# Kernel optimization log

Measured on AMD Instinct MI355X. Metric: run time of the kernel, lower is better.

## Reference

```python
import jax, jax.numpy as jnp
import numpy as np

B, S, D = 2, 2048, 2048
H, KVH, HD = 16, 4, 128
E, TOPK, FF = 8, 2, 4096
EPS = 1e-6
THETA = 1000000.0


def setup_inputs() -> dict:
    key = jax.random.key(0)
    ks = jax.random.split(key, 12)
    s = 0.02
    return {
        'hidden_states': jax.random.normal(ks[0], (B, S, D), jnp.float32),
        'attention_mask': jnp.ones((B, S), dtype=bool),
        'wq': jax.random.normal(ks[1], (D, H * HD), jnp.float32) * s,
        'wk': jax.random.normal(ks[2], (D, KVH * HD), jnp.float32) * s,
        'wv': jax.random.normal(ks[3], (D, KVH * HD), jnp.float32) * s,
        'wo': jax.random.normal(ks[4], (H * HD, D), jnp.float32) * s,
        'ln1_w': jnp.ones((D,), jnp.float32),
        'ln2_w': jnp.ones((D,), jnp.float32),
        'gate_w': jax.random.normal(ks[5], (D, E), jnp.float32) * s,
        'w_gate': jax.random.normal(ks[6], (E, D, FF), jnp.float32) * s,
        'w_up': jax.random.normal(ks[7], (E, D, FF), jnp.float32) * s,
        'w_down': jax.random.normal(ks[8], (E, FF, D), jnp.float32) * s,
    }


def rms_norm(x, w):
    xf = x.astype(jnp.float32)
    var = jnp.mean(jnp.square(xf), axis=-1, keepdims=True)
    return w * (xf * jax.lax.rsqrt(var + EPS)).astype(x.dtype)


def rotate_half(x):
    x1, x2 = x[..., : x.shape[-1] // 2], x[..., x.shape[-1] // 2 :]
    return jnp.concatenate((-x2, x1), axis=-1)


def attention(x, mask, wq, wk, wv, wo):
    q = (x @ wq).reshape(B, S, H, HD)
    k = (x @ wk).reshape(B, S, KVH, HD)
    v = (x @ wv).reshape(B, S, KVH, HD)
    # RoPE (fp32 freqs, as in MixtralRotaryEmbedding)
    inv_freq = 1.0 / (THETA ** (jnp.arange(0, HD, 2, dtype=jnp.float32) / HD))
    freqs = jnp.arange(S, dtype=jnp.float32)[:, None] * inv_freq[None, :]  # [S, HD/2]
    emb = jnp.concatenate([freqs, freqs], axis=-1)  # [S, HD]
    cos = jnp.cos(emb)[None, :, None, :]  # [1,S,1,HD]
    sin = jnp.sin(emb)[None, :, None, :]
    q = q * cos + rotate_half(q) * sin
    k = k * cos + rotate_half(k) * sin
    # GQA: repeat kv heads
    k = jnp.repeat(k, H // KVH, axis=2)
    v = jnp.repeat(v, H // KVH, axis=2)
    # faithful to source: keep-mask is triu(ones, k=1) (strictly-above-diagonal)
    causal = jnp.triu(jnp.ones((S, S), dtype=bool), k=1)
    combined = mask[:, None, None, :] & causal[None, None, :, :]  # [B,1,S,S]
    neg = jnp.finfo(jnp.float32).min
    bias = jnp.where(combined, 0.0, neg).astype(jnp.float32)
    scores = jnp.einsum('bqhd,bkhd->bhqk', q, k) * (HD ** -0.5) + bias
    attn = jax.nn.softmax(scores, axis=-1)
    out = jnp.einsum('bhqk,bkhd->bqhd', attn, v).reshape(B, S, H * HD)
    return out @ wo


def moe(x, gate_w, w_gate, w_up, w_down):
    # x: [T, D]
    T = x.shape[0]
    logits = x.astype(jnp.float32) @ gate_w  # fp32 router, [T, E]
    rw = jax.nn.softmax(logits, axis=-1)
    top_w, top_i = jax.lax.top_k(rw, TOPK)
    top_w = top_w / jnp.sum(top_w, axis=-1, keepdims=True)
    w_full = jnp.zeros((T, E), jnp.float32).at[jnp.arange(T)[:, None], top_i].set(top_w)
    out = jnp.zeros_like(x)
    for e in range(E):  # small fixed expert loop
        h = jax.nn.silu(x @ w_gate[e]) * (x @ w_up[e])
        out = out + w_full[:, e, None] * (h @ w_down[e])
    return out


def reference(hidden_states, attention_mask, wq, wk, wv, wo, ln1_w, ln2_w, gate_w, w_gate, w_up, w_down):
    residual = hidden_states
    h = rms_norm(hidden_states, ln1_w)
    h = residual + attention(h, attention_mask, wq, wk, wv, wo)
    residual = h
    h = rms_norm(h, ln2_w)
    m = moe(h.reshape(-1, D), gate_w, w_gate, w_up, w_down).reshape(B, S, D)
    return residual + m
```

## Files before the change

### kernel.cpp

```cpp
#include <hip/hip_runtime.h>
#include <cstdint>
#include <cstddef>


typedef unsigned short u16;
typedef __attribute__((ext_vector_type(8))) short short8;
typedef __attribute__((ext_vector_type(8))) _Float16 half8;
typedef __attribute__((ext_vector_type(8))) __bf16 bf16x8;
typedef __attribute__((ext_vector_type(4))) float f32x4;
typedef __attribute__((ext_vector_type(4))) u16 us4;
typedef __attribute__((ext_vector_type(4))) unsigned int u32x4;

__device__ __forceinline__ u16 f2bf(float f) {
  unsigned u = __builtin_bit_cast(unsigned, f);
  u += 0x7fffu + ((u >> 16) & 1u);
  return (u16)(u >> 16);
}
__device__ __forceinline__ void splitf16(float x, float scale, u16 &hi, u16 &lo) {
  float xs = x * scale;
  _Float16 h = (_Float16)xs;
  hi = __builtin_bit_cast(u16, h);
  _Float16 l = (_Float16)(xs - (float)h);
  lo = __builtin_bit_cast(u16, l);
}
__device__ __forceinline__ f32x4 mma_bf(short8 a, short8 b, f32x4 c) {
  return __builtin_amdgcn_mfma_f32_16x16x32_bf16(
      __builtin_bit_cast(bf16x8, a), __builtin_bit_cast(bf16x8, b), c, 0, 0, 0);
}
__device__ __forceinline__ f32x4 mma_h(short8 a, short8 b, f32x4 c) {
  return __builtin_amdgcn_mfma_f32_16x16x32_f16(
      __builtin_bit_cast(half8, a), __builtin_bit_cast(half8, b), c, 0, 0, 0);
}
__device__ __forceinline__ void gl16(const u16 *g, u16 *l) {
  __builtin_amdgcn_global_load_lds(
      (const __attribute__((address_space(1))) unsigned *)g,
      (__attribute__((address_space(3))) unsigned *)l, 16, 0, 0);
}

template <int OM>
__global__ __launch_bounds__(256) void k_trans(
    const float *__restrict__ src, u16 *__restrict__ d0, u16 *__restrict__ d1,
    int ld_src, int ld_dst, long long zhi, long long zlo, int zmod,
    long long dstz, int inter, float scale) {
  int z = blockIdx.z;
  src += (long long)(z / zmod) * zhi + (long long)(z % zmod) * zlo;
  d0 += (long long)z * dstz;
  if constexpr (OM == 1) d1 += (long long)z * dstz;
  int r0 = blockIdx.y * 64, c0 = blockIdx.x * 64;
  __shared__ float t[64][65];
  int tx = threadIdx.x;
  int rr = tx >> 4, cc = (tx & 15) * 4;
#pragma unroll
  for (int i = 0; i < 4; i++) {
    float4 v = *(const float4 *)(src + (size_t)(r0 + rr + i * 16) * ld_src + c0 + cc);
    t[rr + i * 16][cc] = v.x; t[rr + i * 16][cc + 1] = v.y;
    t[rr + i * 16][cc + 2] = v.z; t[rr + i * 16][cc + 3] = v.w;
  }
  __syncthreads();
#pragma unroll
  for (int i = 0; i < 4; i++) {
    int c = rr + i * 16;
    int f = c0 + c;
    int drow = (inter < 0) ? f : (((f >> 5) << 6) + (f & 31) + (inter << 5));
    size_t bo = (size_t)drow * ld_dst + r0 + cc;
    if constexpr (OM == 0) {
      us4 o;
#pragma unroll
      for (int j = 0; j < 4; j++) o[j] = f2bf(t[cc + j][c]);
      *(us4 *)(d0 + bo) = o;
    } else {
      us4 oh, ol;
#pragma unroll
      for (int j = 0; j < 4; j++) {
        u16 a, b; splitf16(t[cc + j][c], scale, a, b);
        oh[j] = a; ol[j] = b;
      }
      *(us4 *)(d0 + bo) = oh;
      *(us4 *)(d1 + bo) = ol;
    }
  }
}

__global__ __launch_bounds__(256) void k_rms(
    const float *__restrict__ x, const float *__restrict__ w,
    u16 *__restrict__ oh, u16 *__restrict__ ol, float scale16) {
  int row = blockIdx.x, tid = threadIdx.x;
  const float *xr = x + (size_t)row * 2048;
  float4 v0 = *(const float4 *)(xr + tid * 8);
  float4 v1 = *(const float4 *)(xr + tid * 8 + 4);
  float ss = v0.x * v0.x + v0.y * v0.y + v0.z * v0.z + v0.w * v0.w +
             v1.x * v1.x + v1.y * v1.y + v1.z * v1.z + v1.w * v1.w;
  __shared__ float red[256];
  red[tid] = ss;
  __syncthreads();
  for (int s = 128; s > 0; s >>= 1) {
    if (tid < s) red[tid] += red[tid + s];
    __syncthreads();
  }
  float sc = rsqrtf(red[0] * (1.0f / 2048.0f) + 1e-6f);
  float4 w0 = *(const float4 *)(w + tid * 8);
  float4 w1 = *(const float4 *)(w + tid * 8 + 4);
  float o[8] = {v0.x * sc * w0.x, v0.y * sc * w0.y, v0.z * sc * w0.z, v0.w * sc * w0.w,
                v1.x * sc * w1.x, v1.y * sc * w1.y, v1.z * sc * w1.z, v1.w * sc * w1.w};
  size_t bo = (size_t)row * 2048 + tid * 8;
  if (ol) {
    us4 h0, h1, l0, l1;
#pragma unroll
    for (int j = 0; j < 4; j++) {
      u16 a, b;
      splitf16(o[j], scale16, a, b); h0[j] = a; l0[j] = b;
      splitf16(o[j + 4], scale16, a, b); h1[j] = a; l1[j] = b;
    }
    *(us4 *)(oh + bo) = h0; *(us4 *)(oh + bo + 4) = h1;
    *(us4 *)(ol + bo) = l0; *(us4 *)(ol + bo + 4) = l1;
  } else {
    us4 a, b;
#pragma unroll
    for (int j = 0; j < 4; j++) { a[j] = f2bf(o[j]); b[j] = f2bf(o[j + 4]); }
    *(us4 *)(oh + bo) = a; *(us4 *)(oh + bo + 4) = b;
  }
}

__global__ void k_cs(float2 *__restrict__ cs) {
  int idx = blockIdx.x * 256 + threadIdx.x;
  int s = idx >> 6, i = idx & 63;
  double inv = exp2(-(double)i * (19.931568569324174 / 64.0));
  double ang = (double)s * inv;
  cs[idx] = make_float2((float)cos(ang), (float)sin(ang));
}

__global__ __launch_bounds__(256) void k_rope(
    const float *__restrict__ qkv, const float2 *__restrict__ cs,
    u16 *__restrict__ qh, u16 *__restrict__ ql,
    u16 *__restrict__ kh, u16 *__restrict__ kl) {
  int t = blockIdx.x, tid = threadIdx.x;
  int s = t & 2047;
  const float *bp = qkv + (size_t)t * 3072;
  for (int p = tid; p < 1024; p += 256) {
    int hh = p >> 6, i = p & 63;
    float2 c = cs[s * 64 + i];
    float x1 = bp[hh * 128 + i], x2 = bp[hh * 128 + 64 + i];
    float o1 = x1 * c.x - x2 * c.y, o2 = x2 * c.x + x1 * c.y;
    size_t b1 = (size_t)t * 2048 + hh * 128 + i;
    u16 a, b;
    splitf16(o1, 16.f, a, b); qh[b1] = a; ql[b1] = b;
    splitf16(o2, 16.f, a, b); qh[b1 + 64] = a; ql[b1 + 64] = b;
  }
  {
    int hh = tid >> 6, i = tid & 63;
    float2 c = cs[s * 64 + i];
    float x1 = bp[2048 + hh * 128 + i], x2 = bp[2048 + hh * 128 + 64 + i];
    float o1 = x1 * c.x - x2 * c.y, o2 = x2 * c.x + x1 * c.y;
    size_t b1 = (size_t)t * 512 + hh * 128 + i;
    u16 a, b;
    splitf16(o1, 16.f, a, b); kh[b1] = a; kl[b1] = b;
    splitf16(o2, 16.f, a, b); kh[b1 + 64] = a; kl[b1 + 64] = b;
  }
}

__global__ __launch_bounds__(512, 4) void k_attn(
    const u16 *__restrict__ qh, const u16 *__restrict__ ql,
    const u16 *__restrict__ kh, const u16 *__restrict__ kl,
    const u16 *__restrict__ vh, const u16 *__restrict__ vl,
    u16 *__restrict__ oh, u16 *__restrict__ ol) {
  const int qx = blockIdx.x, kvh = blockIdx.y, b = blockIdx.z;
  const int qt = (b == 0) ? qx : 63 - qx;
  const int q0 = qt * 32;
  const int tid = threadIdx.x, wid = tid >> 6, lane = tid & 63;
  const int hq = wid & 3, rh = wid >> 2;
  const int h = kvh * 4 + hq;
  const int lr = lane & 15, g = lane >> 4, lk = g * 8;
  const float SC = 0.08838834764831845f * 1.44269504088896341f / 256.0f;

  __shared__ alignas(16) u16 KT[2][2][4096];
  __shared__ alignas(16) u16 VT[2][2][4096];
  __shared__ alignas(16) u16 Pb[8][2][512];

  short8 qfh[4], qfl[4];
  {
    size_t qo = (size_t)(b * 2048 + q0 + rh * 16 + lr) * 2048 + h * 128 + lk;
#pragma unroll
    for (int c = 0; c < 4; c++) {
      qfh[c] = *(const short8 *)(qh + qo + c * 32);
      qfl[c] = *(const short8 *)(ql + qo + c * 32);
    }
  }
  f32x4 accO[8] = {};
  float m_r[4], l_r[4];
#pragma unroll
  for (int r = 0; r < 4; r++) { m_r[r] = -3.0e38f; l_r[r] = 0.f; }

  const int kv_start = q0;
  const int nIter = (2048 - kv_start) >> 5;

  const u16 *khp = kh + (size_t)(b * 2048) * 512 + kvh * 128;
  const u16 *klp = kl + (size_t)(b * 2048) * 512 + kvh * 128;
  const u16 *vhp = vh + ((size_t)(b * 4 + kvh) * 128) * 2048;
  const u16 *vlp = vl + ((size_t)(b * 4 + kvh) * 128) * 2048;

  auto stage = [&](int bf, int kv0) {
    const int c0 = wid * 64;
    const int cc = tid;
    const int krow = cc >> 4, kcol = (cc & 15) ^ (krow & 7);
    const size_t kg = (size_t)(kv0 + krow) * 512 + kcol * 8;
    gl16(khp + kg, &KT[bf][0][c0 * 8]);
    gl16(klp + kg, &KT[bf][1][c0 * 8]);
    const int vd = cc >> 2, vi = (cc & 3) ^ (vd & 3);
    const size_t vg = (size_t)vd * 2048 + kv0 + vi * 8;
    gl16(vhp + vg, &VT[bf][0][c0 * 8]);
    gl16(vlp + vg, &VT[bf][1][c0 * 8]);
  };

  stage(0, kv_start);
  __syncthreads();
  int buf = 0;
  for (int it = 0; it < nIter; it++) {
    const int kv0 = kv_start + (it << 5);
    if (it + 1 < nIter) stage(buf ^ 1, kv0 + 32);
    f32x4 s0 = {}, s1 = {};
    {
      const u16 *KhL = KT[buf][0], *KlL = KT[buf][1];
#pragma unroll
      for (int c = 0; c < 4; c++) {
        const int idx0 = lr * 128 + (((c * 4 + g) ^ (lr & 7)) << 3);
        const int idx1 = idx0 + 2048;
        short8 k0h = *(const short8 *)(KhL + idx0);
        short8 k0l = *(const short8 *)(KlL + idx0);
        short8 k1h = *(const short8 *)(KhL + idx1);
        short8 k1l = *(const short8 *)(KlL + idx1);
        s0 = mma_h(qfh[c], k0h, s0); s0 = mma_h(qfh[c], k0l, s0); s0 = mma_h(qfl[c], k0h, s0);
        s1 = mma_h(qfh[c], k1h, s1); s1 = mma_h(qfh[c], k1l, s1); s1 = mma_h(qfl[c], k1h, s1);
      }
    }
    const bool msk = (kv0 <= q0 + 31);
    float alpha[4];
#pragma unroll
    for (int r = 0; r < 4; r++) {
      float v0 = s0[r] * SC, v1 = s1[r] * SC;
      if (msk) {
        int rowq = q0 + rh * 16 + g * 4 + r;
        if (kv0 + lr <= rowq) v0 = -3.0e38f;
        if (kv0 + 16 + lr <= rowq) v1 = -3.0e38f;
      }
      float mx = fmaxf(v0, v1);
#pragma unroll
      for (int o = 1; o < 16; o <<= 1) mx = fmaxf(mx, __shfl_xor(mx, o));
      float mn = fmaxf(m_r[r], mx);
      float p0 = exp2f(v0 - mn), p1 = exp2f(v1 - mn);
      float sum = p0 + p1;
#pragma unroll
      for (int o = 1; o < 16; o <<= 1) sum += __shfl_xor(sum, o);
      alpha[r] = exp2f(m_r[r] - mn);
      l_r[r] = l_r[r] * alpha[r] + sum;
      m_r[r] = mn;
      const int prow = g * 4 + r;
      {
        int c0l = lr, c1l = 16 + lr;
        int p0i = prow * 32 + ((c0l & 7) | ((((c0l >> 3) ^ g) & 3) << 3));
        int p1i = prow * 32 + ((c1l & 7) | ((((c1l >> 3) ^ g) & 3) << 3));
        u16 x, y;
        splitf16(p0, 16.f, x, y); Pb[wid][0][p0i] = x; Pb[wid][1][p0i] = y;
        splitf16(p1, 16.f, x, y); Pb[wid][0][p1i] = x; Pb[wid][1][p1i] = y;
      }
    }
#pragma unroll
    for (int nt = 0; nt < 8; nt++) {
      f32x4 t = accO[nt];
      t[0] *= alpha[0]; t[1] *= alpha[1]; t[2] *= alpha[2]; t[3] *= alpha[3];
      accO[nt] = t;
    }
    asm volatile("s_waitcnt lgkmcnt(0)" ::: "memory");
    const int pidx = lr * 32 + (((g ^ (lr >> 2)) & 3) << 3);
    short8 pfh = *(const short8 *)(&Pb[wid][0][pidx]);
    short8 pfl = *(const short8 *)(&Pb[wid][1][pidx]);
    {
      const u16 *VhL = VT[buf][0], *VlL = VT[buf][1];
#pragma unroll
      for (int nt = 0; nt < 8; nt++) {
        const int d = nt * 16 + lr;
        const int vidx = d * 32 + (((g ^ (d & 3)) & 3) << 3);
        short8 wfh = *(const short8 *)(VhL + vidx);
        short8 wfl = *(const short8 *)(VlL + vidx);
        f32x4 t = accO[nt];
        t = mma_h(pfh, wfh, t); t = mma_h(pfh, wfl, t); t = mma_h(pfl, wfh, t);
        accO[nt] = t;
      }
    }
    __syncthreads();
    buf ^= 1;
  }
  float inv[4];
#pragma unroll
  for (int r = 0; r < 4; r++) inv[r] = 1.0f / (l_r[r] * 256.0f);
#pragma unroll
  for (int nt = 0; nt < 8; nt++)
#pragma unroll
    for (int r = 0; r < 4; r++) {
      float v = accO[nt][r] * inv[r];
      size_t idx = (size_t)(b * 2048 + q0 + rh * 16 + g * 4 + r) * 2048 + h * 128 + nt * 16 + lr;
      u16 x, y; splitf16(v, 16.f, x, y);
      oh[idx] = x; ol[idx] = y;
    }
}

__global__ __launch_bounds__(256) void k_fixrow(
    const u16 *__restrict__ vh, const u16 *__restrict__ vl,
    u16 *__restrict__ oh, u16 *__restrict__ ol) {
  const int bg = blockIdx.x >> 4, dg = blockIdx.x & 15;
  const int tid = threadIdx.x, lane = tid & 63, w = tid >> 6;
  __shared__ float part[4][8];
#pragma unroll
  for (int i = 0; i < 8; i++) {
    size_t ro = ((size_t)(bg * 128 + dg * 8 + i)) * 2048 + tid * 8;
    short8 a = *(const short8 *)(vh + ro);
    short8 c = *(const short8 *)(vl + ro);
    float s = 0.f;
#pragma unroll
    for (int j = 0; j < 8; j++)
      s += (float)__builtin_bit_cast(_Float16, (u16)a[j]) +
           (float)__builtin_bit_cast(_Float16, (u16)c[j]);
#pragma unroll
    for (int o = 1; o < 64; o <<= 1) s += __shfl_xor(s, o);
    if (lane == 0) part[w][i] = s;
  }
  __syncthreads();
  if (tid < 8) {
    float tot = part[0][tid] + part[1][tid] + part[2][tid] + part[3][tid];
    float v = tot * (1.0f / 32768.0f);
    u16 x, y; splitf16(v, 16.f, x, y);
    int bb = bg >> 2, kvh = bg & 3;
#pragma unroll
    for (int hq2 = 0; hq2 < 4; hq2++) {
      size_t idx = ((size_t)(bb * 2048 + 2047)) * 2048 + (kvh * 4 + hq2) * 128 + dg * 8 + tid;
      oh[idx] = x; ol[idx] = y;
    }
  }
}

template <int MODE>
__global__ __launch_bounds__(512, 1) void k_gemmS(
    const u16 *__restrict__ Ah, const u16 *__restrict__ Al,
    const u16 *__restrict__ Bh, const u16 *__restrict__ Bl,
    int K, int lda, int ldb, int ldc, float descale,
    float *__restrict__ outf, const float *__restrict__ resid) {
  const int n0 = blockIdx.x * 128, m0 = blockIdx.y * 128;
  const int tid = threadIdx.x, wid = tid >> 6, lane = tid & 63;
  const int wr = wid >> 2, wc = wid & 3;
  const int l15 = lane & 15, l4 = lane >> 4;

  __shared__ alignas(16) u16 Ls[4][4][4096];

  const int s = wid * 64 + lane;
  const int row = s >> 2;
  const int kc = (s & 3) ^ ((row >> 1) & 3);
  const u16 *pS[4];
  pS[0] = Ah + (size_t)(m0 + row) * lda + kc * 8;
  pS[1] = Al + (size_t)(m0 + row) * lda + kc * 8;
  pS[2] = Bh + (size_t)(n0 + row) * ldb + kc * 8;
  pS[3] = Bl + (size_t)(n0 + row) * ldb + kc * 8;

  int offA[4], offB[2];
#pragma unroll
  for (int mi = 0; mi < 4; mi++) {
    int r = wr * 64 + mi * 16 + l15;
    offA[mi] = (r * 4 + (l4 ^ ((r >> 1) & 3))) << 3;
  }
#pragma unroll
  for (int ni = 0; ni < 2; ni++) {
    int r = wc * 32 + ni * 16 + l15;
    offB[ni] = (r * 4 + (l4 ^ ((r >> 1) & 3))) << 3;
  }

  f32x4 acc[4][2] = {};
  const int nT = K >> 5;
  auto stage = [&](int t, int x) {
    gl16(pS[x] + (t << 5), &Ls[t & 3][x][wid << 9]);
  };
  stage(0, 0); stage(0, 1); stage(0, 2); stage(0, 3);
  stage(1, 0); stage(1, 1); stage(1, 2); stage(1, 3);
  asm volatile("s_waitcnt vmcnt(4)" ::: "memory");
  __builtin_amdgcn_sched_barrier(0);
  __builtin_amdgcn_s_barrier();
  __builtin_amdgcn_sched_barrier(0);

  short8 bh[2], bl[2], ah[2], al[2], ah2[2], al2[2];
  for (int t = 0; t < nT; t++) {
    const u16 *LAh = &Ls[t & 3][0][0], *LAl = &Ls[t & 3][1][0];
    const u16 *LBh = &Ls[t & 3][2][0], *LBl = &Ls[t & 3][3][0];
#pragma unroll
    for (int i = 0; i < 2; i++) {
      bh[i] = *(const short8 *)(LBh + offB[i]);
      bl[i] = *(const short8 *)(LBl + offB[i]);
      ah[i] = *(const short8 *)(LAh + offA[i]);
      al[i] = *(const short8 *)(LAl + offA[i]);
    }
    if (t + 2 < nT) { stage(t + 2, 0); stage(t + 2, 1); }
    asm volatile("s_waitcnt lgkmcnt(0)" ::: "memory");
    __builtin_amdgcn_sched_barrier(0);
    __builtin_amdgcn_s_setprio(1);
#pragma unroll
    for (int mi = 0; mi < 2; mi++)
#pragma unroll
      for (int ni = 0; ni < 2; ni++) {
        f32x4 c = acc[mi][ni];
        c = mma_h(ah[mi], bh[ni], c);
        c = mma_h(ah[mi], bl[ni], c);
        c = mma_h(al[mi], bh[ni], c);
        acc[mi][ni] = c;
      }
    __builtin_amdgcn_s_setprio(0);
#pragma unroll
    for (int i = 0; i < 2; i++) {
      ah2[i] = *(const short8 *)(LAh + offA[2 + i]);
      al2[i] = *(const short8 *)(LAl + offA[2 + i]);
    }
    if (t + 2 < nT) { stage(t + 2, 2); stage(t + 2, 3); }
    asm volatile("s_waitcnt lgkmcnt(0)" ::: "memory");
    __builtin_amdgcn_sched_barrier(0);
    __builtin_amdgcn_s_setprio(1);
#pragma unroll
    for (int mi = 0; mi < 2; mi++)
#pragma unroll
      for (int ni = 0; ni < 2; ni++) {
        f32x4 c = acc[2 + mi][ni];
        c = mma_h(ah2[mi], bh[ni], c);
        c = mma_h(ah2[mi], bl[ni], c);
        c = mma_h(al2[mi], bh[ni], c);
        acc[2 + mi][ni] = c;
      }
    __builtin_amdgcn_s_setprio(0);
    if (t + 1 < nT) {
      if (t + 2 < nT) {
        asm volatile("s_waitcnt vmcnt(4)" ::: "memory");
      } else {
        asm volatile("s_waitcnt vmcnt(0)" ::: "memory");
      }
      __builtin_amdgcn_sched_barrier(0);
      __builtin_amdgcn_s_barrier();
      __builtin_amdgcn_sched_barrier(0);
    }
  }

#pragma unroll
  for (int mi = 0; mi < 4; mi++)
#pragma unroll
    for (int q = 0; q < 4; q++) {
      int rowo = m0 + wr * 64 + mi * 16 + l4 * 4 + q;
      size_t rb = (size_t)rowo * ldc;
#pragma unroll
      for (int ni = 0; ni < 2; ni++) {
        int col = n0 + wc * 32 + ni * 16 + l15;
        float v = acc[mi][ni][q] * descale;
        if constexpr (MODE == 1) v += resid[rb + col];
        outf[rb + col] = v;
      }
    }
}

template <int MODE>
__global__ __launch_bounds__(512, 1) void k_gemm8(
    const u16 *__restrict__ A, const u16 *__restrict__ Ball,
    int N, int K, int lda, int ldb, int ldc,
    float *__restrict__ outf, u16 *__restrict__ outh,
    const int *__restrict__ offs, const int *__restrict__ counts,
    const int *__restrict__ row_token, const float *__restrict__ row_w) {
  const int e = blockIdx.z;
  const int seg = offs[e], cnt = counts[e];
  const int m0 = blockIdx.y * 256;
  if (m0 >= cnt) return;
  const int n0 = blockIdx.x * 256;
  const u16 *B = Ball + (size_t)e * (size_t)N * (size_t)ldb;
  const int tid = threadIdx.x, wid = tid >> 6, lane = tid & 63;
  const int wr = wid >> 2, wc = wid & 3;
  const int l15 = lane & 15, l4 = lane >> 4;

  __shared__ alignas(16) u16 Ls[4][2][8192];

  const u16 *pA[2], *pB[2];
#pragma unroll
  for (int j = 0; j < 2; j++) {
    int s = (wid * 2 + j) * 64 + lane;
    int row = s >> 2;
    int kc = (s & 3) ^ ((row >> 1) & 3);
    int ra = m0 + row; if (ra > cnt - 1) ra = cnt - 1;
    pA[j] = A + (size_t)(seg + ra) * lda + kc * 8;
    pB[j] = B + (size_t)(n0 + row) * ldb + kc * 8;
  }
  int offA[8], offB[4];
#pragma unroll
  for (int mi = 0; mi < 8; mi++) {
    int r = wr * 128 + mi * 16 + l15;
    offA[mi] = (r * 4 + (l4 ^ ((r >> 1) & 3))) << 3;
  }
#pragma unroll
  for (int ni = 0; ni < 4; ni++) {
    int r = wc * 64 + ni * 16 + l15;
    offB[ni] = (r * 4 + (l4 ^ ((r >> 1) & 3))) << 3;
  }

  f32x4 acc[8][4] = {};
  const int nT = K >> 5;
  auto stage = [&](int t, int j) {
    gl16(pA[j] + (t << 5), &Ls[t & 3][0][(wid * 2 + j) << 9]);
    gl16(pB[j] + (t << 5), &Ls[t & 3][1][(wid * 2 + j) << 9]);
  };
  stage(0, 0); stage(0, 1); stage(1, 0); stage(1, 1);
  asm volatile("s_waitcnt vmcnt(4)" ::: "memory");
  __builtin_amdgcn_sched_barrier(0);
  __builtin_amdgcn_s_barrier();
  __builtin_amdgcn_sched_barrier(0);

  short8 bf[4], af0[4], af1[4];
  for (int t = 0; t < nT; t++) {
    const u16 *LA = &Ls[t & 3][0][0], *LB = &Ls[t & 3][1][0];
#pragma unroll
    for (int i = 0; i < 4; i++) bf[i] = *(const short8 *)(LB + offB[i]);
#pragma unroll
    for (int i = 0; i < 4; i++) af0[i] = *(const short8 *)(LA + offA[i]);
    if (t + 2 < nT) stage(t + 2, 0);
    asm volatile("s_waitcnt lgkmcnt(0)" ::: "memory");
    __builtin_amdgcn_sched_barrier(0);
    __builtin_amdgcn_s_setprio(1);
#pragma unroll
    for (int mi = 0; mi < 4; mi++)
#pragma unroll
      for (int ni = 0; ni < 4; ni++)
        acc[mi][ni] = mma_bf(af0[mi], bf[ni], acc[mi][ni]);
    __builtin_amdgcn_s_setprio(0);
#pragma unroll
    for (int i = 0; i < 4; i++) af1[i] = *(const short8 *)(LA + offA[4 + i]);
    if (t + 2 < nT) stage(t + 2, 1);
    asm volatile("s_waitcnt lgkmcnt(0)" ::: "memory");
    __builtin_amdgcn_sched_barrier(0);
    __builtin_amdgcn_s_setprio(1);
#pragma unroll
    for (int mi = 0; mi < 4; mi++)
#pragma unroll
      for (int ni = 0; ni < 4; ni++)
        acc[4 + mi][ni] = mma_bf(af1[mi], bf[ni], acc[4 + mi][ni]);
    __builtin_amdgcn_s_setprio(0);
    if (t + 1 < nT) {
      if (t + 2 < nT) {
        asm volatile("s_waitcnt vmcnt(4)" ::: "memory");
      } else {
        asm volatile("s_waitcnt vmcnt(0)" ::: "memory");
      }
      __builtin_amdgcn_sched_barrier(0);
      __builtin_amdgcn_s_barrier();
      __builtin_amdgcn_sched_barrier(0);
    }
  }

  if constexpr (MODE == 2) {
    const int f0 = (n0 + wc * 64) >> 1;
#pragma unroll
    for (int mi = 0; mi < 8; mi++)
#pragma unroll
      for (int q = 0; q < 4; q++) {
        int rl = m0 + wr * 128 + mi * 16 + l4 * 4 + q;
        if (rl < cnt) {
          size_t rb = (size_t)(seg + rl) * ldc;
#pragma unroll
          for (int nt = 0; nt < 2; nt++) {
            float g = acc[mi][nt][q], u = acc[mi][nt + 2][q];
            float hv = (g / (1.0f + __expf(-g))) * u;
            outh[rb + f0 + nt * 16 + l15] = f2bf(hv);
          }
        }
      }
  } else {
#pragma unroll
    for (int mi = 0; mi < 8; mi++)
#pragma unroll
      for (int q = 0; q < 4; q++) {
        int rl = m0 + wr * 128 + mi * 16 + l4 * 4 + q;
        if (rl < cnt) {
          int tok = row_token[seg + rl];
          float w = row_w[seg + rl];
          size_t rb = (size_t)tok * ldc;
#pragma unroll
          for (int ni = 0; ni < 4; ni++)
            atomicAdd(outf + rb + n0 + wc * 64 + ni * 16 + l15,
                      w * acc[mi][ni][q]);
        }
      }
  }
}

__global__ __launch_bounds__(64) void k_router(
    const float *__restrict__ hb, const float *__restrict__ w2,
    const float *__restrict__ gw, int *__restrict__ topi,
    float *__restrict__ topw, int *__restrict__ counts) {
  const int t = blockIdx.x, lane = threadIdx.x;
  const float *xr = hb + (size_t)t * 2048;
  float xs[32];
  float ss = 0.f;
#pragma unroll
  for (int c = 0; c < 8; c++) {
    float4 v = *(const float4 *)(xr + c * 256 + lane * 4);
    xs[c * 4 + 0] = v.x; xs[c * 4 + 1] = v.y; xs[c * 4 + 2] = v.z; xs[c * 4 + 3] = v.w;
    ss += v.x * v.x + v.y * v.y + v.z * v.z + v.w * v.w;
  }
#pragma unroll
  for (int o = 1; o < 64; o <<= 1) ss += __shfl_xor(ss, o);
  const float sc = rsqrtf(ss * (1.0f / 2048.0f) + 1e-6f);
  float acc[8] = {0, 0, 0, 0, 0, 0, 0, 0};
#pragma unroll
  for (int c = 0; c < 8; c++)
#pragma unroll
    for (int j = 0; j < 4; j++) {
      int d = c * 256 + lane * 4 + j;
      float xn = xs[c * 4 + j] * sc * w2[d];
      float4 g0 = *(const float4 *)(gw + (size_t)d * 8);
      float4 g1 = *(const float4 *)(gw + (size_t)d * 8 + 4);
      acc[0] += xn * g0.x; acc[1] += xn * g0.y; acc[2] += xn * g0.z; acc[3] += xn * g0.w;
      acc[4] += xn * g1.x; acc[5] += xn * g1.y; acc[6] += xn * g1.z; acc[7] += xn * g1.w;
    }
#pragma unroll
  for (int e = 0; e < 8; e++) {
    float v = acc[e];
#pragma unroll
    for (int o = 1; o < 64; o <<= 1) v += __shfl_xor(v, o);
    acc[e] = v;
  }
  if (lane == 0) {
    float mx = acc[0];
#pragma unroll
    for (int e = 1; e < 8; e++) mx = fmaxf(mx, acc[e]);
    float p[8];
#pragma unroll
    for (int e = 0; e < 8; e++) p[e] = __expf(acc[e] - mx);
    int e0 = 0;
#pragma unroll
    for (int e = 1; e < 8; e++) if (p[e] > p[e0]) e0 = e;
    int e1 = (e0 == 0) ? 1 : 0;
#pragma unroll
    for (int e = 0; e < 8; e++) if (e != e0 && p[e] > p[e1]) e1 = e;
    float s2 = p[e0] + p[e1];
    topi[t * 2] = e0; topi[t * 2 + 1] = e1;
    topw[t * 2] = p[e0] / s2; topw[t * 2 + 1] = p[e1] / s2;
    atomicAdd(counts + e0, 1);
    atomicAdd(counts + e1, 1);
  }
}

__global__ void k_zero(int *__restrict__ p) {
  if (threadIdx.x < 8) p[threadIdx.x] = 0;
}
__global__ void k_offsets(const int *__restrict__ counts, int *__restrict__ offs,
                          int *__restrict__ cursors) {
  if (threadIdx.x == 0) {
    int o = 0;
    for (int e = 0; e < 8; e++) { offs[e] = o; o += counts[e]; cursors[e] = 0; }
    offs[8] = o;
  }
}
__global__ __launch_bounds__(256) void k_scatter(
    const int *__restrict__ topi, const float *__restrict__ topw,
    const int *__restrict__ offs, int *__restrict__ cursors,
    int *__restrict__ row_token, float *__restrict__ row_w) {
  int t = blockIdx.x * 256 + threadIdx.x;
  if (t >= 4096) return;
#pragma unroll
  for (int s = 0; s < 2; s++) {
    int e = topi[t * 2 + s];
    int pos = offs[e] + atomicAdd(cursors + e, 1);
    row_token[pos] = t;
    row_w[pos] = topw[t * 2 + s];
  }
}
__global__ __launch_bounds__(256) void k_gather(
    const u16 *__restrict__ h2, const int *__restrict__ row_token,
    u16 *__restrict__ xg) {
  int r = blockIdx.x;
  int t = row_token[r];
  ((u32x4 *)(xg + (size_t)r * 2048))[threadIdx.x] =
      ((const u32x4 *)(h2 + (size_t)t * 2048))[threadIdx.x];
}

extern "C" void kernel_launch(void *const *d_in, const int *in_sizes, int n_in,
                              void *d_out, int out_size, void *d_ws,
                              size_t ws_size, hipStream_t stream) {
  const float *hidden = (const float *)d_in[0];
  const float *wq = (const float *)d_in[2];
  const float *wk = (const float *)d_in[3];
  const float *wv = (const float *)d_in[4];
  const float *wo = (const float *)d_in[5];
  const float *ln1 = (const float *)d_in[6];
  const float *ln2 = (const float *)d_in[7];
  const float *gw = (const float *)d_in[8];
  const float *wg = (const float *)d_in[9];
  const float *wu = (const float *)d_in[10];
  const float *wd = (const float *)d_in[11];
  float *out = (float *)d_out;

  char *base = (char *)d_ws;
  size_t off = 0;
  auto alloc = [&](size_t bytes) -> char * {
    char *p = base + off;
    off += (bytes + 255) & ~(size_t)255;
    return p;
  };
  u16 *wqkvTh = (u16 *)alloc((size_t)3072 * 2048 * 2);
  u16 *wqkvTl = (u16 *)alloc((size_t)3072 * 2048 * 2);
  u16 *woTh = (u16 *)alloc((size_t)2048 * 2048 * 2);
  u16 *woTl = (u16 *)alloc((size_t)2048 * 2048 * 2);
  u16 *wguT = (u16 *)alloc((size_t)8 * 8192 * 2048 * 2);
  u16 *wdT = (u16 *)alloc((size_t)8 * 2048 * 4096 * 2);
  u16 *h1h = (u16 *)alloc((size_t)4096 * 2048 * 2);
  u16 *h1l = (u16 *)alloc((size_t)4096 * 2048 * 2);
  float *qkv = (float *)alloc((size_t)4096 * 3072 * 4);
  u16 *qbh = (u16 *)alloc((size_t)4096 * 2048 * 2);
  u16 *qbl = (u16 *)alloc((size_t)4096 * 2048 * 2);
  u16 *kbh = (u16 *)alloc((size_t)4096 * 512 * 2);
  u16 *kbl = (u16 *)alloc((size_t)4096 * 512 * 2);
  u16 *vth = (u16 *)alloc((size_t)8 * 128 * 2048 * 2);
  u16 *vtl = (u16 *)alloc((size_t)8 * 128 * 2048 * 2);
  float2 *cs = (float2 *)alloc((size_t)2048 * 64 * 8);
  u16 *aoh = (u16 *)alloc((size_t)4096 * 2048 * 2);
  u16 *aol = (u16 *)alloc((size_t)4096 * 2048 * 2);
  u16 *h2 = (u16 *)alloc((size_t)4096 * 2048 * 2);
  int *topi = (int *)alloc(4096 * 2 * 4);
  float *topwt = (float *)alloc(4096 * 2 * 4);
  int *counts = (int *)alloc(64 * 4);
  int *offs = (int *)alloc(64 * 4);
  int *cursors = (int *)alloc(64 * 4);
  int *row_token = (int *)alloc(8192 * 4);
  float *row_w = (float *)alloc(8192 * 4);
  u16 *xg = (u16 *)alloc((size_t)8192 * 2048 * 2);
  u16 *Hb = (u16 *)alloc((size_t)8192 * 4096 * 2);
  if (off > ws_size) return;

  dim3 T256(256), T64(64);
  k_cs<<<dim3(512), T256, 0, stream>>>(cs);
  k_trans<1><<<dim3(32, 32, 1), T256, 0, stream>>>(wq, wqkvTh, wqkvTl, 2048, 2048, 0, 0, 1, 0, -1, 256.f);
  k_trans<1><<<dim3(8, 32, 1), T256, 0, stream>>>(wk, wqkvTh + (size_t)2048 * 2048, wqkvTl + (size_t)2048 * 2048, 512, 2048, 0, 0, 1, 0, -1, 256.f);
  k_trans<1><<<dim3(8, 32, 1), T256, 0, stream>>>(wv, wqkvTh + (size_t)2560 * 2048, wqkvTl + (size_t)2560 * 2048, 512, 2048, 0, 0, 1, 0, -1, 256.f);
  k_trans<1><<<dim3(32, 32, 1), T256, 0, stream>>>(wo, woTh, woTl, 2048, 2048, 0, 0, 1, 0, -1, 256.f);
  k_trans<0><<<dim3(64, 32, 8), T256, 0, stream>>>(wg, wguT, nullptr, 4096, 2048, (long long)2048 * 4096, 0, 1, (long long)8192 * 2048, 0, 1.f);
  k_trans<0><<<dim3(64, 32, 8), T256, 0, stream>>>(wu, wguT, nullptr, 4096, 2048, (long long)2048 * 4096, 0, 1, (long long)8192 * 2048, 1, 1.f);
  k_trans<0><<<dim3(32, 64, 8), T256, 0, stream>>>(wd, wdT, nullptr, 2048, 4096, (long long)4096 * 2048, 0, 1, (long long)2048 * 4096, -1, 1.f);
  k_rms<<<dim3(4096), T256, 0, stream>>>(hidden, ln1, h1h, h1l, 16.f);
  k_gemmS<0><<<dim3(24, 32), dim3(512), 0, stream>>>(
      h1h, h1l, wqkvTh, wqkvTl, 2048, 2048, 2048, 3072,
      1.f / 4096.f, qkv, nullptr);
  k_rope<<<dim3(4096), T256, 0, stream>>>(qkv, cs, qbh, qbl, kbh, kbl);
  k_trans<1><<<dim3(2, 32, 8), T256, 0, stream>>>(qkv + 2560, vth, vtl, 3072, 2048, (long long)2048 * 3072, 128, 4, (long long)128 * 2048, -1, 16.f);
  k_attn<<<dim3(64, 4, 2), dim3(512), 0, stream>>>(qbh, qbl, kbh, kbl, vth, vtl, aoh, aol);
  k_fixrow<<<dim3(128), T256, 0, stream>>>(vth, vtl, aoh, aol);
  k_gemmS<1><<<dim3(16, 32), dim3(512), 0, stream>>>(
      aoh, aol, woTh, woTl, 2048, 2048, 2048, 2048,
      1.f / 4096.f, out, hidden);
  k_rms<<<dim3(4096), T256, 0, stream>>>(out, ln2, h2, nullptr, 1.f);
  k_zero<<<dim3(1), T64, 0, stream>>>(counts);
  k_router<<<dim3(4096), T64, 0, stream>>>(out, ln2, gw, topi, topwt, counts);
  k_offsets<<<dim3(1), dim3(1), 0, stream>>>(counts, offs, cursors);
  k_scatter<<<dim3(16), T256, 0, stream>>>(topi, topwt, offs, cursors, row_token, row_w);
  k_gather<<<dim3(8192), T256, 0, stream>>>(h2, row_token, xg);
  k_gemm8<2><<<dim3(32, 16, 8), dim3(512), 0, stream>>>(
      xg, wguT, 8192, 2048, 2048, 2048, 4096,
      nullptr, Hb, offs, counts, nullptr, nullptr);
  k_gemm8<3><<<dim3(8, 16, 8), dim3(512), 0, stream>>>(
      Hb, wdT, 2048, 4096, 4096, 4096, 2048,
      out, nullptr, offs, counts, row_token, row_w);
  (void)in_sizes; (void)n_in; (void)out_size;
}
```

Measured before the change: 1.535 ms.

## Software-pipeline LDS fragment reads across k-tiles in both GEMM kernels

Restructures the main loops of the split-fp16 GEMM and the bf16 expert GEMM so that LDS reads for the next k-tile's A/B fragments are issued before the current tile's MFMAs. Waits are relaxed from lgkmcnt(0) to lgkmcnt(4) to overlap them. The global-load wait and barrier move to mid-iteration. The aim is to hide LDS read latency behind MFMA work. The cost is more register pressure and a subtler barrier/vmcnt schedule that could introduce races if the counts are wrong.

```diff
diff --git a/kernel.cpp b/kernel.cpp
--- a/kernel.cpp
+++ b/kernel.cpp
@@ -36,6 +36,7 @@
       (const __attribute__((address_space(1))) unsigned *)g,
       (__attribute__((address_space(3))) unsigned *)l, 16, 0, 0);
 }
+#define SB0() __builtin_amdgcn_sched_barrier(0)
 
 template <int OM>
 __global__ __launch_bounds__(256) void k_trans(
@@ -379,24 +380,34 @@
   stage(0, 0); stage(0, 1); stage(0, 2); stage(0, 3);
   stage(1, 0); stage(1, 1); stage(1, 2); stage(1, 3);
   asm volatile("s_waitcnt vmcnt(4)" ::: "memory");
-  __builtin_amdgcn_sched_barrier(0);
+  SB0();
   __builtin_amdgcn_s_barrier();
-  __builtin_amdgcn_sched_barrier(0);
+  SB0();
 
   short8 bh[2], bl[2], ah[2], al[2], ah2[2], al2[2];
+  {
+    const u16 *LAh = &Ls[0][0][0], *LAl = &Ls[0][1][0];
+    const u16 *LBh = &Ls[0][2][0], *LBl = &Ls[0][3][0];
+#pragma unroll
+    for (int i = 0; i < 2; i++) {
+      ah[i] = *(const short8 *)(LAh + offA[i]);
+      al[i] = *(const short8 *)(LAl + offA[i]);
+      bh[i] = *(const short8 *)(LBh + offB[i]);
+      bl[i] = *(const short8 *)(LBl + offB[i]);
+    }
+  }
   for (int t = 0; t < nT; t++) {
     const u16 *LAh = &Ls[t & 3][0][0], *LAl = &Ls[t & 3][1][0];
-    const u16 *LBh = &Ls[t & 3][2][0], *LBl = &Ls[t & 3][3][0];
+    const u16 *LAhn = &Ls[(t + 1) & 3][0][0], *LAln = &Ls[(t + 1) & 3][1][0];
+    const u16 *LBhn = &Ls[(t + 1) & 3][2][0], *LBln = &Ls[(t + 1) & 3][3][0];
 #pragma unroll
     for (int i = 0; i < 2; i++) {
-      bh[i] = *(const short8 *)(LBh + offB[i]);
-      bl[i] = *(const short8 *)(LBl + offB[i]);
-      ah[i] = *(const short8 *)(LAh + offA[i]);
-      al[i] = *(const short8 *)(LAl + offA[i]);
+      ah2[i] = *(const short8 *)(LAh + offA[2 + i]);
+      al2[i] = *(const short8 *)(LAl + offA[2 + i]);
     }
     if (t + 2 < nT) { stage(t + 2, 0); stage(t + 2, 1); }
-    asm volatile("s_waitcnt lgkmcnt(0)" ::: "memory");
-    __builtin_amdgcn_sched_barrier(0);
+    asm volatile("s_waitcnt lgkmcnt(4)" ::: "memory");
+    SB0();
     __builtin_amdgcn_s_setprio(1);
 #pragma unroll
     for (int mi = 0; mi < 2; mi++)
@@ -409,14 +420,24 @@
         acc[mi][ni] = c;
       }
     __builtin_amdgcn_s_setprio(0);
-#pragma unroll
-    for (int i = 0; i < 2; i++) {
-      ah2[i] = *(const short8 *)(LAh + offA[2 + i]);
-      al2[i] = *(const short8 *)(LAl + offA[2 + i]);
+    if (t + 1 < nT) {
+      if (t + 2 < nT) asm volatile("s_waitcnt vmcnt(2)" ::: "memory");
+      else            asm volatile("s_waitcnt vmcnt(0)" ::: "memory");
+      SB0();
+      __builtin_amdgcn_s_barrier();
+      SB0();
+    }
+    if (t + 1 < nT) {
+#pragma unroll
+      for (int i = 0; i < 2; i++) {
+        ah[i] = *(const short8 *)(LAhn + offA[i]);
+        al[i] = *(const short8 *)(LAln + offA[i]);
+      }
     }
     if (t + 2 < nT) { stage(t + 2, 2); stage(t + 2, 3); }
-    asm volatile("s_waitcnt lgkmcnt(0)" ::: "memory");
-    __builtin_amdgcn_sched_barrier(0);
+    if (t + 1 < nT) asm volatile("s_waitcnt lgkmcnt(4)" ::: "memory");
+    else            asm volatile("s_waitcnt lgkmcnt(0)" ::: "memory");
+    SB0();
     __builtin_amdgcn_s_setprio(1);
 #pragma unroll
     for (int mi = 0; mi < 2; mi++)
@@ -430,14 +451,14 @@
       }
     __builtin_amdgcn_s_setprio(0);
     if (t + 1 < nT) {
-      if (t + 2 < nT) {
-        asm volatile("s_waitcnt vmcnt(4)" ::: "memory");
-      } else {
-        asm volatile("s_waitcnt vmcnt(0)" ::: "memory");
-      }
-      __builtin_amdgcn_sched_barrier(0);
+#pragma unroll
+      for (int i = 0; i < 2; i++) {
+        bh[i] = *(const short8 *)(LBhn + offB[i]);
+        bl[i] = *(const short8 *)(LBln + offB[i]);
+      }
+      SB0();
       __builtin_amdgcn_s_barrier();
-      __builtin_amdgcn_sched_barrier(0);
+      SB0();
     }
   }
 
@@ -506,20 +527,26 @@
   };
   stage(0, 0); stage(0, 1); stage(1, 0); stage(1, 1);
   asm volatile("s_waitcnt vmcnt(4)" ::: "memory");
-  __builtin_amdgcn_sched_barrier(0);
+  SB0();
   __builtin_amdgcn_s_barrier();
-  __builtin_amdgcn_sched_barrier(0);
-
-  short8 bf[4], af0[4], af1[4];
+  SB0();
+
+  short8 af0[4], af1[4], bf[4];
+  {
+    const u16 *LA = &Ls[0][0][0], *LB = &Ls[0][1][0];
+#pragma unroll
+    for (int i = 0; i < 4; i++) af0[i] = *(const short8 *)(LA + offA[i]);
+#pragma unroll
+    for (int i = 0; i < 4; i++) bf[i] = *(const short8 *)(LB + offB[i]);
+  }
   for (int t = 0; t < nT; t++) {
-    const u16 *LA = &Ls[t & 3][0][0], *LB = &Ls[t & 3][1][0];
-#pragma unroll
-    for (int i = 0; i < 4; i++) bf[i] = *(const short8 *)(LB + offB[i]);
-#pragma unroll
-    for (int i = 0; i < 4; i++) af0[i] = *(const short8 *)(LA + offA[i]);
+    const u16 *LA = &Ls[t & 3][0][0];
+    const u16 *LAn = &Ls[(t + 1) & 3][0][0], *LBn = &Ls[(t + 1) & 3][1][0];
+#pragma unroll
+    for (int i = 0; i < 4; i++) af1[i] = *(const short8 *)(LA + offA[4 + i]);
     if (t + 2 < nT) stage(t + 2, 0);
-    asm volatile("s_waitcnt lgkmcnt(0)" ::: "memory");
-    __builtin_amdgcn_sched_barrier(0);
+    asm volatile("s_waitcnt lgkmcnt(4)" ::: "memory");
+    SB0();
     __builtin_amdgcn_s_setprio(1);
 #pragma unroll
     for (int mi = 0; mi < 4; mi++)
@@ -527,11 +554,21 @@
       for (int ni = 0; ni < 4; ni++)
         acc[mi][ni] = mma_bf(af0[mi], bf[ni], acc[mi][ni]);
     __builtin_amdgcn_s_setprio(0);
-#pragma unroll
-    for (int i = 0; i < 4; i++) af1[i] = *(const short8 *)(LA + offA[4 + i]);
+    if (t + 1 < nT) {
+      if (t + 2 < nT) asm volatile("s_waitcnt vmcnt(2)" ::: "memory");
+      else            asm volatile("s_waitcnt vmcnt(0)" ::: "memory");
+      SB0();
+      __builtin_amdgcn_s_barrier();
+      SB0();
+    }
+    if (t + 1 < nT) {
+#pragma unroll
+      for (int i = 0; i < 4; i++) af0[i] = *(const short8 *)(LAn + offA[i]);
+    }
     if (t + 2 < nT) stage(t + 2, 1);
-    asm volatile("s_waitcnt lgkmcnt(0)" ::: "memory");
-    __builtin_amdgcn_sched_barrier(0);
+    if (t + 1 < nT) asm volatile("s_waitcnt lgkmcnt(4)" ::: "memory");
+    else            asm volatile("s_waitcnt lgkmcnt(0)" ::: "memory");
+    SB0();
     __builtin_amdgcn_s_setprio(1);
 #pragma unroll
     for (int mi = 0; mi < 4; mi++)
@@ -540,14 +577,11 @@
         acc[4 + mi][ni] = mma_bf(af1[mi], bf[ni], acc[4 + mi][ni]);
     __builtin_amdgcn_s_setprio(0);
     if (t + 1 < nT) {
-      if (t + 2 < nT) {
-        asm volatile("s_waitcnt vmcnt(4)" ::: "memory");
-      } else {
-        asm volatile("s_waitcnt vmcnt(0)" ::: "memory");
-      }
-      __builtin_amdgcn_sched_barrier(0);
+#pragma unroll
+      for (int i = 0; i < 4; i++) bf[i] = *(const short8 *)(LBn + offB[i]);
+      SB0();
       __builtin_amdgcn_s_barrier();
-      __builtin_amdgcn_sched_barrier(0);
+      SB0();
     }
   }
 
```

Measured after the change: 1.545 ms. Within noise of the previous version (+0.6%).
